# Kernel optimization log

Hardware: AMD Instinct MI355X
Metric: run time of the kernel (lower is better)

Reference implementation:

```python
import jax, jax.numpy as jnp
import numpy as np

BETA = 0.25
DECAY = 0.99
USAGE_DECAY = 0.99
EPS = 1e-5
RESET_THRESHOLD = 100.0


def _sqdist(x, e):
    # squared euclidean distances [N, K]; argmin identical to cdist argmin
    x2 = jnp.sum(x * x, axis=1, keepdims=True)           # [N,1]
    e2 = jnp.sum(e * e, axis=1)[None, :]                 # [1,K]
    return x2 - 2.0 * (x @ e.T) + e2


def setup_inputs() -> dict:
    key = jax.random.key(0)
    ks = jax.random.split(key, 7)
    N, K, D = 32768, 4096, 256
    return {
        "x": jax.random.normal(ks[0], (N, D), jnp.float32),
        "embedding": jax.random.normal(ks[1], (K, D), jnp.float32) * (1.0 / K),
        "ema_cluster_size": jax.random.uniform(ks[2], (K,), jnp.float32),
        "ema_w": jax.random.normal(ks[3], (K, D), jnp.float32) * (1.0 / K),
        "codebook_usage": jax.random.uniform(ks[4], (K,), jnp.float32),
        "steps_since_used": jax.random.randint(ks[5], (K,), 0, 200, jnp.int32),
        "random_indices": jax.random.randint(ks[6], (K,), 0, N, jnp.int32),
    }


def reference(x, embedding, ema_cluster_size, ema_w, codebook_usage,
              steps_since_used, random_indices):
    N, D = x.shape
    K = embedding.shape[0]

    # --- nearest-code lookup ---
    d2 = _sqdist(x, embedding)                 # [N,K]
    indices = jnp.argmin(d2, axis=1)           # [N]
    q = jnp.take(embedding, indices, axis=0)   # [N,D]
    quantized = x + jax.lax.stop_gradient(q - x)

    commitment_loss = jnp.mean((x - jax.lax.stop_gradient(quantized)) ** 2)
    loss = BETA * commitment_loss

    # --- EMA codebook update (encodings.sum(0) and encodings.T @ x as segment sums) ---
    counts = jax.ops.segment_sum(jnp.ones((N,), x.dtype), indices, num_segments=K)
    dw = jax.ops.segment_sum(x, indices, num_segments=K)        # [K,D]
    new_cs = ema_cluster_size * DECAY + (1.0 - DECAY) * counts
    new_ema_w = ema_w * DECAY + (1.0 - DECAY) * dw
    n = jnp.sum(new_cs)
    cluster_size = (new_cs + EPS) / (n + K * EPS) * n
    new_embedding = new_ema_w / cluster_size[:, None]
    new_usage = codebook_usage * USAGE_DECAY + (1.0 - USAGE_DECAY) * counts

    # --- dead-code reset (uses the EMA-updated codebook, as in the original) ---
    idx2 = jnp.argmin(_sqdist(x, new_embedding), axis=1)
    used = jax.ops.segment_sum(jnp.ones((N,), x.dtype), idx2, num_segments=K) > 0
    steps = jnp.where(used, 0.0, steps_since_used.astype(x.dtype) + 1.0)
    dead = steps > RESET_THRESHOLD
    replacement = jnp.take(x, random_indices, axis=0)           # [K,D]
    new_embedding = jnp.where(dead[:, None], replacement, new_embedding)
    steps = jnp.where(dead, 0.0, steps)

    usage_rate = jnp.mean((new_usage > 0).astype(x.dtype))

    return (quantized, indices, loss, new_embedding, new_cs, new_ema_w,
            new_usage, steps, usage_rate)
```

## Files before the change

### kernel.cpp

```cpp
#include <hip/hip_runtime.h>
#include <math.h>

typedef float vf4 __attribute__((ext_vector_type(4)));
typedef _Float16 f16;
typedef _Float16 f16x8 __attribute__((ext_vector_type(8)));
typedef _Float16 f16x4 __attribute__((ext_vector_type(4)));
typedef float f32x4 __attribute__((ext_vector_type(4)));

static constexpr int Ncnt = 32768;
static constexpr int Kcb  = 4096;
static constexpr int Dim  = 256;

static constexpr float EPSf  = 1e-5f;
static constexpr float KEPSf = (float)(4096.0 * 1e-5);

static constexpr size_t OQ  = 0;
static constexpr size_t OI  = (size_t)Ncnt * Dim;
static constexpr size_t OL  = OI + Ncnt;
static constexpr size_t OE  = OL + 1;
static constexpr size_t OCS = OE + (size_t)Kcb * Dim;
static constexpr size_t OW  = OCS + Kcb;
static constexpr size_t OU  = OW + (size_t)Kcb * Dim;
static constexpr size_t OS  = OU + Kcb;
static constexpr size_t OR  = OS + Kcb;

#define GLD16(gp, lp)                                                   \
  __builtin_amdgcn_global_load_lds(                                     \
      (const __attribute__((address_space(1))) void*)(gp),              \
      (__attribute__((address_space(3))) void*)(lp), 16, 0, 0)

__device__ __forceinline__ float np_sq256(const float* __restrict__ p) {
  float tot[2];
  #pragma unroll
  for (int h = 0; h < 2; ++h) {
    const float* a = p + h * 128;
    float r[8];
    #pragma unroll
    for (int j = 0; j < 8; ++j) r[j] = __fmul_rn(a[j], a[j]);
    for (int i = 8; i < 128; i += 8)
      #pragma unroll
      for (int j = 0; j < 8; ++j) r[j] = __fadd_rn(r[j], __fmul_rn(a[i + j], a[i + j]));
    tot[h] = __fadd_rn(__fadd_rn(__fadd_rn(r[0], r[1]), __fadd_rn(r[2], r[3])),
                       __fadd_rn(__fadd_rn(r[4], r[5]), __fadd_rn(r[6], r[7])));
  }
  return __fadd_rn(tot[0], tot[1]);
}

__global__ void rowsq_np(const float* __restrict__ E, float* __restrict__ e2, int rows) {
  const int k = blockIdx.x * 256 + threadIdx.x;
  if (k < rows) e2[k] = np_sq256(E + (size_t)k * Dim);
}

__global__ void split_rows(const float* __restrict__ src, f16* __restrict__ dst,
                           const float scale, const int rows)
{
  const int i   = blockIdx.x * 256 + threadIdx.x;
  const int row = i >> 6;
  const int d0  = (i & 63) * 4;
  if (row >= rows) return;
  const vf4 v = *(const vf4*)(src + (size_t)row * 256 + d0);
  f16x4 hi, lo;
  #pragma unroll
  for (int j = 0; j < 4; ++j) {
    const float t = __fmul_rn(v[j], scale);
    const f16 h   = (f16)t;
    const float r = __fsub_rn(t, (float)h);
    hi[j] = h;
    lo[j] = (f16)r;
  }
  *(f16x4*)(dst + (size_t)row * 512 + d0)       = hi;
  *(f16x4*)(dst + (size_t)row * 512 + 256 + d0) = lo;
}

#define AOF(s) ((((s) >> 3) == 1 ? 256 : 0) + ((s) & 7) * 32)
#define BOF(s) ((((s) >> 3) == 2 ? 256 : 0) + ((s) & 7) * 32)
#define STAGE4(aP0, aP1, bP0, bP1, bufi)                                \
  do {                                                                  \
    GLD16((aP0), &As[(bufi)][wv * 1024]);                               \
    GLD16((aP1), &As[(bufi)][wv * 1024 + 512]);                         \
    GLD16((bP0), &Bs[(bufi)][wv * 1024]);                               \
    GLD16((bP1), &Bs[(bufi)][wv * 1024 + 512]);                         \
  } while (0)

__global__ __launch_bounds__(256, 2) void mfma_argmin(
    const f16* __restrict__ Xs, const f16* __restrict__ Es,
    const float* __restrict__ e2, const float two_scale,
    int* __restrict__ cand)
{
  __shared__ __align__(16) f16 As[3][128 * 32];
  __shared__ __align__(16) f16 Bs[3][128 * 32];

  const int tid  = threadIdx.x;
  const int bid  = blockIdx.x;
  const int row0 = (bid >> 3) * 128;
  const int cg   = bid & 7;
  const int colbase = cg * 512;

  const int l  = tid & 63;
  const int wv = tid >> 6;
  const int wr = wv >> 1;
  const int wc = wv & 1;
  const int lc = l & 15;
  const int kc = l >> 4;

  const int srow = wv * 32 + (l >> 2);
  const int chs  = (l & 3) ^ ((l >> 3) & 3);

  const f16* aB0 = Xs + (size_t)(row0 + srow) * 512 + chs * 8;
  const f16* aB1 = aB0 + 16 * 512;
  const f16* bBase0 = Es + (size_t)(colbase + srow) * 512 + chs * 8;
  const f16* bBase1 = bBase0 + 16 * 512;

  const int ks = (kc ^ ((lc >> 1) & 3)) * 8;

  const float nts = -two_scale;

  float t1[16], t2[16];
  int   i1[16], i2[16];
  #pragma unroll
  for (int s = 0; s < 16; ++s) {
    t1[s] = INFINITY; t2[s] = INFINITY; i1[s] = 0x7fffffff; i2[s] = 0x7fffffff;
  }

  STAGE4(aB0 + AOF(0), aB1 + AOF(0), bBase0 + BOF(0), bBase1 + BOF(0), 0);
  STAGE4(aB0 + AOF(1), aB1 + AOF(1), bBase0 + BOF(1), bBase1 + BOF(1), 1);

  #pragma unroll 1
  for (int ct = 0; ct < 4; ++ct) {
    const f16* bC0 = bBase0 + ct * 65536;
    const f16* bC1 = bBase1 + ct * 65536;

    f32x4 acc[4][4];
    #pragma unroll
    for (int i = 0; i < 4; ++i)
      #pragma unroll
      for (int j = 0; j < 4; ++j)
        acc[i][j] = (f32x4){0.0f, 0.0f, 0.0f, 0.0f};

    #pragma unroll
    for (int st = 0; st < 24; ++st) {
      if (st == 23) { asm volatile("s_waitcnt vmcnt(0)" ::: "memory"); }
      else          { asm volatile("s_waitcnt vmcnt(4)" ::: "memory"); }
      __builtin_amdgcn_s_barrier();
      __builtin_amdgcn_sched_barrier(0);

      const int cur = st % 3;
      f16x8 af[4], bf[4];
      #pragma unroll
      for (int f = 0; f < 4; ++f) {
        af[f] = *(const f16x8*)(&As[cur][(wr * 64 + f * 16 + lc) * 32 + ks]);
        bf[f] = *(const f16x8*)(&Bs[cur][(wc * 64 + f * 16 + lc) * 32 + ks]);
      }

      if (st + 2 < 24) {
        STAGE4(aB0 + AOF(st + 2), aB1 + AOF(st + 2),
               bC0 + BOF(st + 2), bC1 + BOF(st + 2), (st + 2) % 3);
      } else if (ct < 3) {
        STAGE4(aB0 + AOF(st - 22), aB1 + AOF(st - 22),
               bC0 + 65536 + BOF(st - 22), bC1 + 65536 + BOF(st - 22),
               (st + 2) % 3);
      }

      __builtin_amdgcn_s_setprio(1);
      #pragma unroll
      for (int fm = 0; fm < 4; ++fm)
        #pragma unroll
        for (int fn = 0; fn < 4; ++fn)
          acc[fm][fn] = __builtin_amdgcn_mfma_f32_16x16x32_f16(
              af[fm], bf[fn], acc[fm][fn], 0, 0, 0);
      __builtin_amdgcn_s_setprio(0);
    }

    float e2v[4];
    #pragma unroll
    for (int fn = 0; fn < 4; ++fn)
      e2v[fn] = e2[colbase + ct * 128 + wc * 64 + fn * 16 + lc];

    #pragma unroll
    for (int fm = 0; fm < 4; ++fm) {
      #pragma unroll
      for (int j = 0; j < 4; ++j) {
        const int s = fm * 4 + j;
        #pragma unroll
        for (int fn = 0; fn < 4; ++fn) {
          const int col = colbase + ct * 128 + wc * 64 + fn * 16 + lc;
          const float t = fmaf(nts, acc[fm][fn][j], e2v[fn]);
          if (t < t1[s]) {
            t2[s] = t1[s]; i2[s] = i1[s]; t1[s] = t; i1[s] = col;
          } else if (t < t2[s]) {
            t2[s] = t; i2[s] = col;
          }
        }
      }
    }
  }

  #pragma unroll
  for (int s = 0; s < 16; ++s) {
    #pragma unroll
    for (int m = 1; m < 16; m <<= 1) {
      const float p1 = __shfl_xor(t1[s], m);
      const float p2 = __shfl_xor(t2[s], m);
      const int   q1 = __shfl_xor(i1[s], m);
      const int   q2 = __shfl_xor(i2[s], m);
      const bool pl = (p1 < t1[s]) || (p1 == t1[s] && q1 < i1[s]);
      float n1, n2; int m1, m2;
      if (pl) {
        n1 = p1; m1 = q1;
        const bool sl = (t1[s] < p2) || (t1[s] == p2 && i1[s] < q2);
        n2 = sl ? t1[s] : p2; m2 = sl ? i1[s] : q2;
      } else {
        n1 = t1[s]; m1 = i1[s];
        const bool sl = (p1 < t2[s]) || (p1 == t2[s] && q1 < i2[s]);
        n2 = sl ? p1 : t2[s]; m2 = sl ? q1 : i2[s];
      }
      t1[s] = n1; i1[s] = m1; t2[s] = n2; i2[s] = m2;
    }
  }

  if (lc == 0) {
    #pragma unroll
    for (int fm = 0; fm < 4; ++fm)
      #pragma unroll
      for (int j = 0; j < 4; ++j) {
        const int s    = fm * 4 + j;
        const int rloc = wr * 64 + fm * 16 + kc * 4 + j;
        const size_t base = ((size_t)(row0 + rloc) * 8 + cg) * 4 + wc * 2;
        cand[base]     = i1[s];
        cand[base + 1] = i2[s];
      }
  }
}

__global__ void recheck(const float* __restrict__ X, const float* __restrict__ x2g,
                        const float* __restrict__ Eref, const float* __restrict__ e2ref,
                        const int* __restrict__ cand, int* __restrict__ idxo)
{
  __shared__ float Xl[8][256];
  const int tid  = threadIdx.x;
  const int rg   = tid >> 5;
  const int lr   = tid & 31;
  const int row0 = blockIdx.x * 8;
  const int row  = row0 + rg;

  {
    const float* xp = X + (size_t)row * 256 + lr * 8;
    *(vf4*)(&Xl[rg][lr * 8])     = *(const vf4*)xp;
    *(vf4*)(&Xl[rg][lr * 8 + 4]) = *(const vf4*)(xp + 4);
  }
  __syncthreads();

  int k = cand[(size_t)row * 32 + lr];

  float acc = 0.0f;
  const float* ep = Eref + (size_t)k * 256;
  for (int d4 = 0; d4 < 64; ++d4) {
    const vf4 xv = *(const vf4*)(&Xl[rg][d4 * 4]);
    const vf4 ev = *(const vf4*)(ep + d4 * 4);
    acc = fmaf(xv[0], ev[0], acc);
    acc = fmaf(xv[1], ev[1], acc);
    acc = fmaf(xv[2], ev[2], acc);
    acc = fmaf(xv[3], ev[3], acc);
  }
  float s = __fadd_rn(__fsub_rn(x2g[row], __fmul_rn(2.0f, acc)), e2ref[k]);

  #pragma unroll
  for (int m = 1; m < 32; m <<= 1) {
    const float os = __shfl_xor(s, m);
    const int   ok = __shfl_xor(k, m);
    if (os < s || (os == s && ok < k)) { s = os; k = ok; }
  }
  if (lr == 0) idxo[row] = k;
}

__global__ void stats_cd(const float* __restrict__ X, const float* __restrict__ E,
                         const int* __restrict__ idx, float* __restrict__ counts,
                         float* __restrict__ dw, double* __restrict__ loss_acc)
{
  __shared__ double part[4];
  const int tid  = threadIdx.x;
  const int lane = tid & 63, w = tid >> 6;
  const int row  = blockIdx.x * 4 + w;
  const int k    = idx[row];
  const vf4 xv = ((const vf4*)X)[(size_t)row * 64 + lane];
  const vf4 qv = ((const vf4*)E)[(size_t)k * 64 + lane];
  const float d0 = xv[0]-qv[0], d1 = xv[1]-qv[1], d2 = xv[2]-qv[2], d3 = xv[3]-qv[3];
  double ps = (double)(d0*d0 + d1*d1 + d2*d2 + d3*d3);
  #pragma unroll
  for (int o = 32; o; o >>= 1) ps += __shfl_down(ps, o);
  #pragma unroll
  for (int j = 0; j < 4; ++j)
    atomicAdd(dw + (size_t)k * Dim + lane * 4 + j, xv[j]);
  if (lane == 0) {
    part[w] = ps;
    atomicAdd(counts + k, 1.0f);
  }
  __syncthreads();
  if (tid == 0) atomicAdd(loss_acc, part[0] + part[1] + part[2] + part[3]);
}

__global__ void gather_q(const float* __restrict__ E, const int* __restrict__ idx,
                         float* __restrict__ out)
{
  const int tid  = threadIdx.x;
  const int lane = tid & 63, w = tid >> 6;
  const int row  = blockIdx.x * 4 + w;
  const int k    = idx[row];
  ((vf4*)out)[(size_t)row * 64 + lane] = ((const vf4*)E)[(size_t)k * 64 + lane];
  if (lane == 0) out[OI + row] = (float)k;
}

__global__ void cs_usage(const float* __restrict__ ecs, const float* __restrict__ usage,
                         const float* __restrict__ counts, float* __restrict__ out,
                         int* __restrict__ pos_cnt)
{
  __shared__ int si[256];
  const int tid = threadIdx.x;
  const int k   = blockIdx.x * 256 + tid;
  const float cnt = counts[k];
  const float ncs = __fadd_rn(__fmul_rn(ecs[k], 0.99f), __fmul_rn(0.01f, cnt));
  out[OCS + k] = ncs;
  const float nus = __fadd_rn(__fmul_rn(usage[k], 0.99f), __fmul_rn(0.01f, cnt));
  out[OU + k] = nus;
  si[tid] = (nus > 0.0f) ? 1 : 0;
  __syncthreads();
  for (int s = 128; s; s >>= 1) {
    if (tid < s) si[tid] += si[tid + s];
    __syncthreads();
  }
  if (tid == 0) atomicAdd(pos_cnt, si[0]);
}

__global__ void n_np_kernel(const float* __restrict__ ncs, float* __restrict__ nf) {
  __shared__ float leaf[32];
  const int t = threadIdx.x;
  if (t < 32) {
    const float* a = ncs + t * 128;
    float r[8];
    #pragma unroll
    for (int j = 0; j < 8; ++j) r[j] = a[j];
    for (int i = 8; i < 128; i += 8)
      #pragma unroll
      for (int j = 0; j < 8; ++j) r[j] = __fadd_rn(r[j], a[i + j]);
    leaf[t] = __fadd_rn(__fadd_rn(__fadd_rn(r[0], r[1]), __fadd_rn(r[2], r[3])),
                        __fadd_rn(__fadd_rn(r[4], r[5]), __fadd_rn(r[6], r[7])));
  }
  __syncthreads();
  if (t == 0) {
    float v[32];
    #pragma unroll
    for (int i = 0; i < 32; ++i) v[i] = leaf[i];
    for (int n = 32; n > 1; n >>= 1)
      for (int i = 0; i < (n >> 1); ++i) v[i] = __fadd_rn(v[2 * i], v[2 * i + 1]);
    *nf = v[0];
  }
}

__global__ void emb_pre(const float* __restrict__ emaw, float* __restrict__ out,
                        const float* __restrict__ nf)
{
  const int k = blockIdx.x;
  const int d = threadIdx.x;
  const size_t o = (size_t)k * Dim + d;
  const float dwv = out[OW + o];
  const float w = __fadd_rn(__fmul_rn(emaw[o], 0.99f), __fmul_rn(0.01f, dwv));
  out[OW + o] = w;
  const float nv  = *nf;
  const float ncs = out[OCS + k];
  const float cs  = __fmul_rn(__fdiv_rn(__fadd_rn(ncs, EPSf), __fadd_rn(nv, KEPSf)), nv);
  out[OE + o] = __fdiv_rn(w, cs);
}

__global__ void used_scatter(const int* __restrict__ idx2, int* __restrict__ used) {
  const int i = blockIdx.x * 256 + threadIdx.x;
  used[idx2[i]] = 1;
}

__global__ void finalize_k(const float* __restrict__ X, const int* __restrict__ used,
                           const int* __restrict__ steps_in, const int* __restrict__ rnd,
                           float* __restrict__ out)
{
  const int k = blockIdx.x, d = threadIdx.x;
  const int u = used[k];
  const float st = u ? 0.0f : (float)steps_in[k] + 1.0f;
  const bool dead = st > 100.0f;
  if (dead) out[OE + (size_t)k * Dim + d] = X[(size_t)rnd[k] * Dim + d];
  if (d == 0) out[OS + k] = dead ? 0.0f : st;
}

__global__ void write_scalars(const double* __restrict__ loss_acc,
                              const int* __restrict__ pos_cnt, float* __restrict__ out)
{
  if (threadIdx.x == 0) {
    out[OL] = 0.25f * (float)(*loss_acc / (double)((size_t)Ncnt * Dim));
    out[OR] = (float)(*pos_cnt) / (float)Kcb;
  }
}

extern "C" void kernel_launch(void* const* d_in, const int* in_sizes, int n_in,
                              void* d_out, int out_size, void* d_ws, size_t ws_size,
                              hipStream_t stream)
{
  const float* X     = (const float*)d_in[0];
  const float* E     = (const float*)d_in[1];
  const float* ECS   = (const float*)d_in[2];
  const float* EMAW  = (const float*)d_in[3];
  const float* USAGE = (const float*)d_in[4];
  const int*   STEPS = (const int*)d_in[5];
  const int*   RND   = (const int*)d_in[6];
  float* out = (float*)d_out;

  float* wsf = (float*)d_ws;
  float*  counts   = wsf;
  int*    used     = (int*)(wsf + 4096);
  double* loss_acc = (double*)(wsf + 8192);
  float*  nf       = wsf + 8194;
  int*    pos_cnt  = (int*)(wsf + 8195);
  const size_t ZN  = 8200;
  float* x2g  = wsf + 8320;
  float* e2   = wsf + 41088;
  float* e2p  = wsf + 45184;
  int*   idx1 = (int*)(wsf + 49280);
  int*   idx2 = (int*)(wsf + 82048);
  f16*   Es   = (f16*)(wsf + 114816);
  int*   cand = (int*)(wsf + 1163392);
  f16*   Xsp  = (f16*)out;

  hipMemsetAsync(d_ws, 0, ZN * sizeof(float), stream);
  hipMemsetAsync(out + OW, 0, (size_t)Kcb * Dim * sizeof(float), stream);

  rowsq_np     <<<Ncnt / 256, 256, 0, stream>>>(X, x2g, Ncnt);
  rowsq_np     <<<Kcb / 256,  256, 0, stream>>>(E, e2, Kcb);
  split_rows   <<<Ncnt / 4,   256, 0, stream>>>(X, Xsp, 64.0f, Ncnt);
  split_rows   <<<Kcb / 4,    256, 0, stream>>>(E, Es, 16777216.0f, Kcb);
  mfma_argmin  <<<2048,       256, 0, stream>>>(Xsp, Es, e2, 0x1p-29f, cand);
  recheck      <<<Ncnt / 8,   256, 0, stream>>>(X, x2g, E, e2, cand, idx1);
  stats_cd     <<<Ncnt / 4,   256, 0, stream>>>(X, E, idx1, counts, out + OW, loss_acc);
  cs_usage     <<<Kcb / 256,  256, 0, stream>>>(ECS, USAGE, counts, out, pos_cnt);
  n_np_kernel  <<<1,          64,  0, stream>>>(out + OCS, nf);
  emb_pre      <<<Kcb,        256, 0, stream>>>(EMAW, out, nf);
  rowsq_np     <<<Kcb / 256,  256, 0, stream>>>(out + OE, e2p, Kcb);
  split_rows   <<<Kcb / 4,    256, 0, stream>>>(out + OE, Es, 256.0f, Kcb);
  mfma_argmin  <<<2048,       256, 0, stream>>>(Xsp, Es, e2p, 0x1p-13f, cand);
  recheck      <<<Ncnt / 8,   256, 0, stream>>>(X, x2g, out + OE, e2p, cand, idx2);
  used_scatter <<<Ncnt / 256, 256, 0, stream>>>(idx2, used);
  finalize_k   <<<Kcb,        256, 0, stream>>>(X, used, STEPS, RND, out);
  gather_q     <<<Ncnt / 4,   256, 0, stream>>>(E, idx1, out);
  write_scalars<<<1,          64,  0, stream>>>(loss_acc, pos_cnt, out);

  (void)in_sizes; (void)n_in; (void)out_size; (void)ws_size;
}
```

Baseline: 1.858 ms.

## Move per-row top-2 argmin state from registers to LDS, raise occupancy

```diff
diff --git a/kernel.cpp b/kernel.cpp
--- a/kernel.cpp
+++ b/kernel.cpp
@@ -82,13 +82,15 @@
     GLD16((bP1), &Bs[(bufi)][wv * 1024 + 512]);                         \
   } while (0)
 
-__global__ __launch_bounds__(256, 2) void mfma_argmin(
+__global__ __launch_bounds__(256, 3) void mfma_argmin(
     const f16* __restrict__ Xs, const f16* __restrict__ Es,
     const float* __restrict__ e2, const float two_scale,
     int* __restrict__ cand)
 {
   __shared__ __align__(16) f16 As[3][128 * 32];
   __shared__ __align__(16) f16 Bs[3][128 * 32];
+  __shared__ float bT[128][2][2];
+  __shared__ int   bI[128][2][2];
 
   const int tid  = threadIdx.x;
   const int bid  = blockIdx.x;
@@ -103,6 +105,10 @@
   const int lc = l & 15;
   const int kc = l >> 4;
 
+  bT[wr * 64 + l][wc][0] = INFINITY;  bT[wr * 64 + l][wc][1] = INFINITY;
+  bI[wr * 64 + l][wc][0] = 0x7fffffff; bI[wr * 64 + l][wc][1] = 0x7fffffff;
+  asm volatile("s_waitcnt lgkmcnt(0)" ::: "memory");
+
   const int srow = wv * 32 + (l >> 2);
   const int chs  = (l & 3) ^ ((l >> 3) & 3);
 
@@ -114,13 +120,6 @@
   const int ks = (kc ^ ((lc >> 1) & 3)) * 8;
 
   const float nts = -two_scale;
-
-  float t1[16], t2[16];
-  int   i1[16], i2[16];
-  #pragma unroll
-  for (int s = 0; s < 16; ++s) {
-    t1[s] = INFINITY; t2[s] = INFINITY; i1[s] = 0x7fffffff; i2[s] = 0x7fffffff;
-  }
 
   STAGE4(aB0 + AOF(0), aB1 + AOF(0), bBase0 + BOF(0), bBase1 + BOF(0), 0);
   STAGE4(aB0 + AOF(1), aB1 + AOF(1), bBase0 + BOF(1), bBase1 + BOF(1), 1);
@@ -180,55 +179,63 @@
     for (int fm = 0; fm < 4; ++fm) {
       #pragma unroll
       for (int j = 0; j < 4; ++j) {
-        const int s = fm * 4 + j;
+        float u1 = INFINITY, u2 = INFINITY;
+        int   v1 = 0x7fffffff, v2 = 0x7fffffff;
         #pragma unroll
         for (int fn = 0; fn < 4; ++fn) {
           const int col = colbase + ct * 128 + wc * 64 + fn * 16 + lc;
           const float t = fmaf(nts, acc[fm][fn][j], e2v[fn]);
-          if (t < t1[s]) {
-            t2[s] = t1[s]; i2[s] = i1[s]; t1[s] = t; i1[s] = col;
-          } else if (t < t2[s]) {
-            t2[s] = t; i2[s] = col;
+          if (t < u1) { u2 = u1; v2 = v1; u1 = t; v1 = col; }
+          else if (t < u2) { u2 = t; v2 = col; }
+        }
+        #pragma unroll
+        for (int m = 1; m < 16; m <<= 1) {
+          const float p1 = __shfl_xor(u1, m);
+          const float p2 = __shfl_xor(u2, m);
+          const int   q1 = __shfl_xor(v1, m);
+          const int   q2 = __shfl_xor(v2, m);
+          const bool pl = (p1 < u1) || (p1 == u1 && q1 < v1);
+          float n1, n2; int m1, m2;
+          if (pl) {
+            n1 = p1; m1 = q1;
+            const bool sl = (u1 < p2) || (u1 == p2 && v1 < q2);
+            n2 = sl ? u1 : p2; m2 = sl ? v1 : q2;
+          } else {
+            n1 = u1; m1 = v1;
+            const bool sl = (p1 < u2) || (p1 == u2 && q1 < v2);
+            n2 = sl ? p1 : u2; m2 = sl ? q1 : v2;
           }
+          u1 = n1; v1 = m1; u2 = n2; v2 = m2;
+        }
+        if (lc == 0) {
+          const int rloc = wr * 64 + fm * 16 + kc * 4 + j;
+          const float c1 = bT[rloc][wc][0], c2 = bT[rloc][wc][1];
+          const int   d1 = bI[rloc][wc][0], d2 = bI[rloc][wc][1];
+          const bool fn_ = (u1 < c1) || (u1 == c1 && v1 < d1);
+          float r1, r2; int s1, s2;
+          if (fn_) {
+            r1 = u1; s1 = v1;
+            const bool sl = (u2 < c1) || (u2 == c1 && v2 < d1);
+            r2 = sl ? u2 : c1; s2 = sl ? v2 : d1;
+          } else {
+            r1 = c1; s1 = d1;
+            const bool sl = (c2 < u1) || (c2 == u1 && d2 < v1);
+            r2 = sl ? c2 : u1; s2 = sl ? d2 : v1;
+          }
+          bT[rloc][wc][0] = r1; bT[rloc][wc][1] = r2;
+          bI[rloc][wc][0] = s1; bI[rloc][wc][1] = s2;
         }
       }
     }
   }
 
-  #pragma unroll
-  for (int s = 0; s < 16; ++s) {
-    #pragma unroll
-    for (int m = 1; m < 16; m <<= 1) {
-      const float p1 = __shfl_xor(t1[s], m);
-      const float p2 = __shfl_xor(t2[s], m);
-      const int   q1 = __shfl_xor(i1[s], m);
-      const int   q2 = __shfl_xor(i2[s], m);
-      const bool pl = (p1 < t1[s]) || (p1 == t1[s] && q1 < i1[s]);
-      float n1, n2; int m1, m2;
-      if (pl) {
-        n1 = p1; m1 = q1;
-        const bool sl = (t1[s] < p2) || (t1[s] == p2 && i1[s] < q2);
-        n2 = sl ? t1[s] : p2; m2 = sl ? i1[s] : q2;
-      } else {
-        n1 = t1[s]; m1 = i1[s];
-        const bool sl = (p1 < t2[s]) || (p1 == t2[s] && q1 < i2[s]);
-        n2 = sl ? p1 : t2[s]; m2 = sl ? q1 : i2[s];
-      }
-      t1[s] = n1; i1[s] = m1; t2[s] = n2; i2[s] = m2;
-    }
-  }
-
-  if (lc == 0) {
-    #pragma unroll
-    for (int fm = 0; fm < 4; ++fm)
-      #pragma unroll
-      for (int j = 0; j < 4; ++j) {
-        const int s    = fm * 4 + j;
-        const int rloc = wr * 64 + fm * 16 + kc * 4 + j;
-        const size_t base = ((size_t)(row0 + rloc) * 8 + cg) * 4 + wc * 2;
-        cand[base]     = i1[s];
-        cand[base + 1] = i2[s];
-      }
+  __syncthreads();
+  if (tid < 128) {
+    const size_t base = ((size_t)(row0 + tid) * 8 + cg) * 4;
+    cand[base]     = bI[tid][0][0];
+    cand[base + 1] = bI[tid][0][1];
+    cand[base + 2] = bI[tid][1][0];
+    cand[base + 3] = bI[tid][1][1];
   }
 }
 
```

Result: faster. 1.719 ms (-7.5%).
